# Kernel tuning notes

Measured on AMD Instinct MI355X. Metric: run time of the kernel, lower is better.

## Reference

```python
import math
import jax, jax.numpy as jnp
import numpy as np

S, B, H = 2048, 1, 4096
NH, HD = 32, 128          # heads, head dim
ROT = HD // 2             # rotary dim per 2D-RoPE half = 64


def rotate_half(x):
    x1, x2 = jnp.split(x, 2, axis=-1)
    return jnp.concatenate([-x2, x1], axis=-1)


def rope_tables(seq_len, dim, base=10000.0):
    inv_freq = 1.0 / (base ** (jnp.arange(0, dim, 2, dtype=jnp.float32) / dim))
    freqs = jnp.arange(seq_len, dtype=jnp.float32)[:, None] * inv_freq[None, :]
    emb = jnp.concatenate([freqs, freqs], axis=-1)  # [S, dim]
    return jnp.cos(emb), jnp.sin(emb)


def apply_rope(q, k, cos, sin, pos):
    # q,k: [S,B,NH,ROT]; pos: [S,B] -> gather cos/sin per token
    c = cos[pos][:, :, None, :]  # [S,B,1,ROT]
    s = sin[pos][:, :, None, :]
    return q * c + rotate_half(q) * s, k * c + rotate_half(k) * s


def setup_inputs() -> dict:
    key = jax.random.key(0)
    ks = jax.random.split(key, 5)
    hidden_states = jax.random.normal(ks[0], (S, B, H), dtype=jnp.float32)
    pos = jnp.arange(S, dtype=jnp.int64 if jax.config.jax_enable_x64 else jnp.int32)
    position_ids = jnp.stack([pos, pos])[None]  # [B=1, 2, S]
    attention_mask = jnp.triu(jnp.ones((S, S), dtype=bool), k=1)[None, None]  # True = masked
    scale = 0.02
    wqkv = jax.random.normal(ks[1], (3 * H, H), dtype=jnp.float32) * scale
    bqkv = jax.random.normal(ks[2], (3 * H,), dtype=jnp.float32) * scale
    wdense = jax.random.normal(ks[3], (H, H), dtype=jnp.float32) * scale
    bdense = jax.random.normal(ks[4], (H,), dtype=jnp.float32) * scale
    return {"hidden_states": hidden_states, "position_ids": position_ids,
            "attention_mask": attention_mask, "wqkv": wqkv, "bqkv": bqkv,
            "wdense": wdense, "bdense": bdense, "layer_id": 1}


def reference(hidden_states, position_ids, attention_mask, wqkv, bqkv, wdense, bdense, layer_id):
    s, b, h = hidden_states.shape
    # fused QKV projection: [S,B,NH,3*HD]
    mixed = (jnp.einsum('sbh,oh->sbo', hidden_states, wqkv) + bqkv).reshape(s, b, NH, 3 * HD)
    q, k, v = jnp.split(mixed, 3, axis=-1)  # each [S,B,NH,HD]

    # 2D RoPE: split head dim in half, rotate each half with its own position ids
    q1, q2 = jnp.split(q, 2, axis=-1)
    k1, k2 = jnp.split(k, 2, axis=-1)
    cos, sin = rope_tables(s, ROT)
    pos = position_ids[:, 0, :].T       # [S,B]
    block_pos = position_ids[:, 1, :].T  # [S,B]
    q1, k1 = apply_rope(q1, k1, cos, sin, pos)
    q2, k2 = apply_rope(q2, k2, cos, sin, block_pos)
    q = jnp.concatenate([q1, q2], axis=-1)
    k = jnp.concatenate([k1, k2], axis=-1)

    # layer-scaled attention (ChatGLM style)
    coeff = float(layer_id + 1)
    q = q / (math.sqrt(HD) * coeff)
    scores = jnp.einsum('sbhd,tbhd->bhst', q, k)  # [B,NH,S,S]
    scores = jnp.where(attention_mask, jnp.float32(-10000.0), scores)
    scores = scores.astype(jnp.float32) * coeff
    probs = jax.nn.softmax(scores, axis=-1).astype(q.dtype)
    context = jnp.einsum('bhst,tbhd->sbhd', probs, v).reshape(s, b, h)

    out = jnp.einsum('sbh,oh->sbo', context, wdense) + bdense
    return out
```

## Files before the change

### kernel.cpp

```cpp
#include <hip/hip_runtime.h>

typedef unsigned short u16;
typedef unsigned int u32;
typedef __attribute__((ext_vector_type(4))) float f32x4;
typedef __attribute__((ext_vector_type(16))) float f32x16;
typedef __attribute__((ext_vector_type(8))) short bf16x8;
typedef __attribute__((ext_vector_type(2))) unsigned int u32x2;

#define S_LEN 2048
#define NHEAD 32
#define HDD 128
#define HID 4096
#define N_QKV 12288
#define KDIM 4096
#define RS 12288

__device__ __forceinline__ u16 f2bf(float f) {
  u32 u = __builtin_bit_cast(u32, f);
  u = (u + 0x7FFFu + ((u >> 16) & 1u)) >> 16;
  return (u16)u;
}
__device__ __forceinline__ float bf2f(u16 h) {
  u32 u = ((u32)h) << 16;
  return __builtin_bit_cast(float, u);
}

__device__ __forceinline__ int gkey(int line) { return (line ^ (line >> 1)) & 7; }

__device__ __forceinline__ void gl2lds16(const void* g, void* l) {
  __builtin_amdgcn_global_load_lds(
      (const __attribute__((address_space(1))) u32*)g,
      (__attribute__((address_space(3))) u32*)l, 16, 0, 0);
}

#define FULL_BAR()                          \
  {                                         \
    asm volatile("" ::: "memory");          \
    __builtin_amdgcn_s_barrier();           \
    asm volatile("" ::: "memory");          \
  }

__global__ __launch_bounds__(256) void cvt3_kernel(const float* __restrict__ s0, u16* __restrict__ d0, int n0,
                                                   const float* __restrict__ s2, u16* __restrict__ d2, int n2,
                                                   float* __restrict__ cos_t, float* __restrict__ sin_t) {
  int i = blockIdx.x * blockDim.x + threadIdx.x;
  if (i < S_LEN * 32) {
    int s = i >> 5, ii = i & 31;
    float invf = expf(-0.28782313662425572f * (float)ii);
    float a = (float)s * invf;
    cos_t[i] = cosf(a);
    sin_t[i] = sinf(a);
  }
  int st = gridDim.x * blockDim.x;
  int ntot = n0 + n2;
  for (; i < ntot; i += st) {
    const float* s;
    u16* d;
    int j = i;
    if (j < n0) {
      s = s0; d = d0;
    } else {
      j -= n0; s = s2; d = d2;
    }
    float4 v = ((const float4*)s)[j];
    u32x2 o;
    o.x = (u32)f2bf(v.x) | ((u32)f2bf(v.y) << 16);
    o.y = (u32)f2bf(v.z) | ((u32)f2bf(v.w) << 16);
    ((u32x2*)d)[j] = o;
  }
}

__global__ __launch_bounds__(256) void ropek_kernel(u16* __restrict__ mixed,
                                                    const int* __restrict__ pid,
                                                    const float* __restrict__ cos_t,
                                                    const float* __restrict__ sin_t) {
  int idx = blockIdx.x * blockDim.x + threadIdx.x;
  const int total = NHEAD * S_LEN * 2 * 8;
  if (idx >= total) return;
  int j = idx & 7;
  int half = (idx >> 3) & 1;
  int s = (idx >> 4) & (S_LEN - 1);
  int h = idx >> 15;
  int i0 = j * 4;
  int p = pid[half * S_LEN + s];
  float4 c4 = *(const float4*)(cos_t + p * 32 + i0);
  float4 s4 = *(const float4*)(sin_t + p * 32 + i0);
  u16* base = mixed + (size_t)s * RS + h * 384 + 128 + half * 64 + i0;
  ushort4 x1v = *(const ushort4*)(base);
  ushort4 x2v = *(const ushort4*)(base + 32);
  ushort4 o1, o2;
  {
    float x1 = bf2f(x1v.x), x2 = bf2f(x2v.x);
    o1.x = f2bf(x1 * c4.x - x2 * s4.x);
    o2.x = f2bf(x2 * c4.x + x1 * s4.x);
  }
  {
    float x1 = bf2f(x1v.y), x2 = bf2f(x2v.y);
    o1.y = f2bf(x1 * c4.y - x2 * s4.y);
    o2.y = f2bf(x2 * c4.y + x1 * s4.y);
  }
  {
    float x1 = bf2f(x1v.z), x2 = bf2f(x2v.z);
    o1.z = f2bf(x1 * c4.z - x2 * s4.z);
    o2.z = f2bf(x2 * c4.z + x1 * s4.z);
  }
  {
    float x1 = bf2f(x1v.w), x2 = bf2f(x2v.w);
    o1.w = f2bf(x1 * c4.w - x2 * s4.w);
    o2.w = f2bf(x2 * c4.w + x1 * s4.w);
  }
  *(ushort4*)(base) = o1;
  *(ushort4*)(base + 32) = o2;
}

__global__ __launch_bounds__(512, 2) void gemmQ(const u16* __restrict__ A,
                                                const u16* __restrict__ B,
                                                const float* __restrict__ bias,
                                                u16* __restrict__ outb) {
  __shared__ __align__(16) char lds[3][40960];

  const int tid = threadIdx.x;
  const int lane = tid & 63, w = tid >> 6;
  const int l31 = lane & 31, hh = lane >> 5;
  const int wm = w >> 2, wn = w & 3;

  int x = blockIdx.x & 7, loc = blockIdx.x >> 3;
  int mb = loc & 7, nb = x * 4 + (loc >> 3);
  const int bm = mb * 256, bn = nb * 384;

  f32x16 acc[4][3];
#pragma unroll
  for (int mi = 0; mi < 4; ++mi)
#pragma unroll
    for (int ni = 0; ni < 3; ++ni)
#pragma unroll
      for (int r = 0; r < 16; ++r) acc[mi][ni][r] = 0.f;

  const size_t K2 = (size_t)KDIM * 2;

  const char* gA[2];
#pragma unroll
  for (int j = 0; j < 2; ++j) {
    int slot = j * 512 + tid;
    int line = slot >> 3;
    int sl = (slot & 7) ^ gkey(line);
    int row = 2 * line + (sl >> 2);
    int colb = (sl & 3) * 16;
    gA[j] = (const char*)A + (size_t)(bm + row) * K2 + colb;
  }
  const char* gB[3];
#pragma unroll
  for (int j = 0; j < 3; ++j) {
    int slot = j * 512 + tid;
    int line = slot >> 3;
    int sl = (slot & 7) ^ gkey(line);
    int row = 2 * line + (sl >> 2);
    int colb = (sl & 3) * 16;
    gB[j] = (const char*)B + (size_t)(bn + row) * K2 + colb;
  }
  const int ldst = w * 1024;

#define QIA(t, bi)                                                  \
  {                                                                 \
    char* Lb = lds[bi];                                             \
    gl2lds16(gA[0] + (size_t)(t) * 64, Lb + ldst);                  \
    gl2lds16(gA[1] + (size_t)(t) * 64, Lb + 8192 + ldst);           \
  }
#define QIB(t, bi)                                                  \
  {                                                                 \
    char* Lb = lds[bi] + 16384;                                     \
    _Pragma("unroll")                                               \
    for (int j = 0; j < 3; ++j)                                     \
      gl2lds16(gB[j] + (size_t)(t) * 64, Lb + j * 8192 + ldst);     \
  }

  int offA[4][2], offB[3][2];
#pragma unroll
  for (int mi = 0; mi < 4; ++mi) {
    int r = wm * 128 + mi * 32 + l31;
    int line = r >> 1;
#pragma unroll
    for (int kk = 0; kk < 2; ++kk) {
      int sl = (((r & 1) << 2) + kk * 2 + hh) ^ gkey(line);
      offA[mi][kk] = line * 128 + sl * 16;
    }
  }
#pragma unroll
  for (int ni = 0; ni < 3; ++ni) {
    int r = wn * 96 + ni * 32 + l31;
    int line = r >> 1;
#pragma unroll
    for (int kk = 0; kk < 2; ++kk) {
      int sl = (((r & 1) << 2) + kk * 2 + hh) ^ gkey(line);
      offB[ni][kk] = 16384 + line * 128 + sl * 16;
    }
  }

  QIA(0, 0); QIB(0, 0);
  QIA(1, 1); QIB(1, 1);
  asm volatile("s_waitcnt vmcnt(5)" ::: "memory");
  FULL_BAR();

  int cur = 0, nx2 = 2;
  for (int kt = 0; kt < 128; ++kt) {
    const char* buf = lds[cur];
    const bool pf = (kt + 2) < 128;
    bf16x8 a[4], b[3];
#pragma unroll
    for (int mi = 0; mi < 4; ++mi) a[mi] = *(const bf16x8*)(buf + offA[mi][0]);
#pragma unroll
    for (int ni = 0; ni < 3; ++ni) b[ni] = *(const bf16x8*)(buf + offB[ni][0]);
    if (pf) QIA(kt + 2, nx2);
    FULL_BAR();
    __builtin_amdgcn_s_setprio(1);
#pragma unroll
    for (int mi = 0; mi < 4; ++mi)
#pragma unroll
      for (int ni = 0; ni < 3; ++ni)
        acc[mi][ni] = __builtin_amdgcn_mfma_f32_32x32x16_bf16(a[mi], b[ni], acc[mi][ni], 0, 0, 0);
    __builtin_amdgcn_s_setprio(0);
#pragma unroll
    for (int mi = 0; mi < 4; ++mi) a[mi] = *(const bf16x8*)(buf + offA[mi][1]);
#pragma unroll
    for (int ni = 0; ni < 3; ++ni) b[ni] = *(const bf16x8*)(buf + offB[ni][1]);
    if (pf) {
      QIB(kt + 2, nx2);
      asm volatile("s_waitcnt vmcnt(5)" ::: "memory");
    } else if (kt == 126) {
      asm volatile("s_waitcnt vmcnt(0)" ::: "memory");
    }
    FULL_BAR();
    __builtin_amdgcn_s_setprio(1);
#pragma unroll
    for (int mi = 0; mi < 4; ++mi)
#pragma unroll
      for (int ni = 0; ni < 3; ++ni)
        acc[mi][ni] = __builtin_amdgcn_mfma_f32_32x32x16_bf16(a[mi], b[ni], acc[mi][ni], 0, 0, 0);
    __builtin_amdgcn_s_setprio(0);
    cur = (cur + 1 == 3) ? 0 : cur + 1;
    nx2 = (nx2 + 1 == 3) ? 0 : nx2 + 1;
  }
#undef QIA
#undef QIB

#pragma unroll
  for (int ni = 0; ni < 3; ++ni) {
    int n = bn + wn * 96 + ni * 32 + l31;
    float bv = bias[n];
#pragma unroll
    for (int mi = 0; mi < 4; ++mi) {
      int m0 = bm + wm * 128 + mi * 32 + 4 * hh;
#pragma unroll
      for (int reg = 0; reg < 16; ++reg) {
        int row = m0 + (reg & 3) + 8 * (reg >> 2);
        outb[(size_t)row * N_QKV + n] = f2bf(acc[mi][ni][reg] + bv);
      }
    }
  }
}

__global__ __launch_bounds__(512, 2) void gemmD(const u16* __restrict__ A,
                                                const float* __restrict__ Bf,
                                                const float* __restrict__ bias,
                                                float* __restrict__ outf) {
  __shared__ __align__(16) char lds[2][49152];

  const int tid = threadIdx.x;
  const int lane = tid & 63, w = tid >> 6;
  const int l31 = lane & 31, hh = lane >> 5;
  const int wm = w >> 1, wn = w & 1;

  int x = blockIdx.x & 7, loc = blockIdx.x >> 3;
  int mb = loc & 7, nb = x * 4 + (loc >> 3);
  const int bm = mb * 256, bn = nb * 128;

  f32x16 acc[2][2];
#pragma unroll
  for (int mi = 0; mi < 2; ++mi)
#pragma unroll
    for (int ni = 0; ni < 2; ++ni)
#pragma unroll
      for (int r = 0; r < 16; ++r) acc[mi][ni][r] = 0.f;

  const size_t K2 = (size_t)KDIM * 2;

  const char* gA[2];
#pragma unroll
  for (int j = 0; j < 2; ++j) {
    int slot = j * 512 + tid;
    int line = slot >> 3;
    int sl = (slot & 7) ^ gkey(line);
    int row = 2 * line + (sl >> 2);
    int colb = (sl & 3) * 16;
    gA[j] = (const char*)A + (size_t)(bm + row) * K2 + colb;
  }
  int bline = tid >> 3;
  int bsl = tid & 7;
  int brow = 2 * bline + (bsl >> 2);
  int bcole = (bsl & 3) * 8;
  const float* gBs = Bf + (size_t)(bn + brow) * KDIM + bcole;
  int bphys = bsl ^ gkey(bline);
  const int bwr = 32768 + bline * 128 + bphys * 16;
  const int ldst = w * 1024;

#define DIA(t, kk)                                                            \
  {                                                                           \
    char* Lb = lds[(t) & 1] + (kk) * 16384;                                   \
    gl2lds16(gA[0] + (size_t)(t) * 128 + (kk) * 64, Lb + ldst);               \
    gl2lds16(gA[1] + (size_t)(t) * 128 + (kk) * 64, Lb + 8192 + ldst);        \
  }
#define DGB(t)                                                                \
  {                                                                           \
    const float* p0 = gBs + (size_t)(t) * 64;                                 \
    b0a = *(const float4*)(p0);                                               \
    b0b = *(const float4*)(p0 + 4);                                           \
    b1a = *(const float4*)(p0 + 32);                                          \
    b1b = *(const float4*)(p0 + 36);                                          \
  }
#define DWB(t)                                                                \
  {                                                                           \
    bf16x8 o0, o1;                                                            \
    o0[0] = (short)f2bf(b0a.x); o0[1] = (short)f2bf(b0a.y);                   \
    o0[2] = (short)f2bf(b0a.z); o0[3] = (short)f2bf(b0a.w);                   \
    o0[4] = (short)f2bf(b0b.x); o0[5] = (short)f2bf(b0b.y);                   \
    o0[6] = (short)f2bf(b0b.z); o0[7] = (short)f2bf(b0b.w);                   \
    o1[0] = (short)f2bf(b1a.x); o1[1] = (short)f2bf(b1a.y);                   \
    o1[2] = (short)f2bf(b1a.z); o1[3] = (short)f2bf(b1a.w);                   \
    o1[4] = (short)f2bf(b1b.x); o1[5] = (short)f2bf(b1b.y);                   \
    o1[6] = (short)f2bf(b1b.z); o1[7] = (short)f2bf(b1b.w);                   \
    char* Lb = lds[(t) & 1];                                                  \
    *(bf16x8*)(Lb + bwr) = o0;                                                \
    *(bf16x8*)(Lb + 8192 + bwr) = o1;                                         \
  }

  int offA[2][2][2], offB[2][2][2];
#pragma unroll
  for (int mi = 0; mi < 2; ++mi) {
    int r = wm * 64 + mi * 32 + l31;
    int line = r >> 1;
#pragma unroll
    for (int kku = 0; kku < 2; ++kku)
#pragma unroll
      for (int st = 0; st < 2; ++st) {
        int sl = (((r & 1) << 2) + st * 2 + hh) ^ gkey(line);
        offA[mi][kku][st] = kku * 16384 + line * 128 + sl * 16;
      }
  }
#pragma unroll
  for (int ni = 0; ni < 2; ++ni) {
    int r = wn * 64 + ni * 32 + l31;
    int line = r >> 1;
#pragma unroll
    for (int kku = 0; kku < 2; ++kku)
#pragma unroll
      for (int st = 0; st < 2; ++st) {
        int sl = (((r & 1) << 2) + st * 2 + hh) ^ gkey(line);
        offB[ni][kku][st] = 32768 + kku * 8192 + line * 128 + sl * 16;
      }
  }

  float4 b0a, b0b, b1a, b1b;
  DGB(0);
  DIA(0, 0);
  DIA(0, 1);
  asm volatile("s_waitcnt vmcnt(4)" ::: "memory");
  DWB(0);
  asm volatile("s_waitcnt vmcnt(0) lgkmcnt(0)" ::: "memory");
  FULL_BAR();

  for (int kt = 0; kt < 64; ++kt) {
    const char* buf = lds[kt & 1];
    const bool pf = (kt + 1) < 64;
    bf16x8 a[2][2], b[2][2];
#pragma unroll
    for (int mi = 0; mi < 2; ++mi)
#pragma unroll
      for (int st = 0; st < 2; ++st) a[mi][st] = *(const bf16x8*)(buf + offA[mi][0][st]);
#pragma unroll
    for (int ni = 0; ni < 2; ++ni)
#pragma unroll
      for (int st = 0; st < 2; ++st) b[ni][st] = *(const bf16x8*)(buf + offB[ni][0][st]);
    if (pf) {
      DIA(kt + 1, 0);
      DGB(kt + 1);
      asm volatile("s_waitcnt vmcnt(6)" ::: "memory");
    } else {
      asm volatile("s_waitcnt vmcnt(0)" ::: "memory");
    }
    FULL_BAR();
    __builtin_amdgcn_s_setprio(1);
#pragma unroll
    for (int st = 0; st < 2; ++st)
#pragma unroll
      for (int mi = 0; mi < 2; ++mi)
#pragma unroll
        for (int ni = 0; ni < 2; ++ni)
          acc[mi][ni] = __builtin_amdgcn_mfma_f32_32x32x16_bf16(a[mi][st], b[ni][st], acc[mi][ni], 0, 0, 0);
    __builtin_amdgcn_s_setprio(0);
#pragma unroll
    for (int mi = 0; mi < 2; ++mi)
#pragma unroll
      for (int st = 0; st < 2; ++st) a[mi][st] = *(const bf16x8*)(buf + offA[mi][1][st]);
#pragma unroll
    for (int ni = 0; ni < 2; ++ni)
#pragma unroll
      for (int st = 0; st < 2; ++st) b[ni][st] = *(const bf16x8*)(buf + offB[ni][1][st]);
    if (pf) {
      DIA(kt + 1, 1);
      asm volatile("s_waitcnt vmcnt(2)" ::: "memory");
      DWB(kt + 1);
      asm volatile("s_waitcnt lgkmcnt(0)" ::: "memory");
    }
    FULL_BAR();
    __builtin_amdgcn_s_setprio(1);
#pragma unroll
    for (int st = 0; st < 2; ++st)
#pragma unroll
      for (int mi = 0; mi < 2; ++mi)
#pragma unroll
        for (int ni = 0; ni < 2; ++ni)
          acc[mi][ni] = __builtin_amdgcn_mfma_f32_32x32x16_bf16(a[mi][st], b[ni][st], acc[mi][ni], 0, 0, 0);
    __builtin_amdgcn_s_setprio(0);
  }
#undef DIA
#undef DGB
#undef DWB

#pragma unroll
  for (int ni = 0; ni < 2; ++ni) {
    int n = bn + wn * 64 + ni * 32 + l31;
    float bv = bias[n];
#pragma unroll
    for (int mi = 0; mi < 2; ++mi) {
      int m0 = bm + wm * 64 + mi * 32 + 4 * hh;
#pragma unroll
      for (int reg = 0; reg < 16; ++reg) {
        int row = m0 + (reg & 3) + 8 * (reg >> 2);
        outf[(size_t)row * HID + n] = acc[mi][ni][reg] + bv;
      }
    }
  }
}

__global__ __launch_bounds__(256) void attn_kernel(const u16* __restrict__ mixed,
                                                   const int* __restrict__ pid,
                                                   const float* __restrict__ cos_t,
                                                   const float* __restrict__ sin_t,
                                                   u16* __restrict__ ctx) {
  __shared__ __align__(16) u16 Ksh[64 * 136];
  __shared__ __align__(16) u16 Vsh[128 * 64];
  __shared__ __align__(16) u16 Pt[4][16 * 72];

  int tid = threadIdx.x;
  int lane = tid & 63, w = tid >> 6;
  int lane15 = lane & 15, g = lane >> 4;

  int bpair = blockIdx.x & 15;
  int h = blockIdx.x >> 4;

  const u16* qp = mixed + (size_t)h * 384;
  const u16* kp = mixed + (size_t)h * 384 + 128;
  const u16* vp = mixed + (size_t)h * 384 + 256;

  int krow = tid >> 2, kc = (tid & 3) * 32;
  int vk0 = 2 * (tid & 31), vd0 = (tid >> 5) * 16;
  f32x4 z4 = {0.f, 0.f, 0.f, 0.f};
  const float QSC = 0.08838834764831845f;
  const float L2E = 1.4426950408889634f;

  for (int pass = 0; pass < 2; ++pass) {
    int qi = pass ? (31 - bpair) : bpair;
    int qbase = qi * 64;
    int qrow = qbase + w * 16 + lane15;
    int ntiles = qi + 1;

    bf16x8 qf[4];
    const u16* qptr = qp + (size_t)qrow * RS + g * 8;
#pragma unroll
    for (int d0 = 0; d0 < 4; ++d0) qf[d0] = *(const bf16x8*)(qptr + d0 * 32);
    {
      int p1 = pid[qrow], p2 = pid[S_LEN + qrow];
      float cc[8], ss[8], dd[8], tt[8];
#pragma unroll
      for (int j = 0; j < 8; ++j) {
        cc[j] = cos_t[p1 * 32 + g * 8 + j];
        ss[j] = sin_t[p1 * 32 + g * 8 + j];
        dd[j] = cos_t[p2 * 32 + g * 8 + j];
        tt[j] = sin_t[p2 * 32 + g * 8 + j];
      }
#pragma unroll
      for (int j = 0; j < 8; ++j) {
        float x1 = bf2f((u16)qf[0][j]), x2 = bf2f((u16)qf[1][j]);
        qf[0][j] = (short)f2bf((x1 * cc[j] - x2 * ss[j]) * QSC);
        qf[1][j] = (short)f2bf((x2 * cc[j] + x1 * ss[j]) * QSC);
        float y1 = bf2f((u16)qf[2][j]), y2 = bf2f((u16)qf[3][j]);
        qf[2][j] = (short)f2bf((y1 * dd[j] - y2 * tt[j]) * QSC);
        qf[3][j] = (short)f2bf((y2 * dd[j] + y1 * tt[j]) * QSC);
      }
    }

    f32x4 pv[8];
#pragma unroll
    for (int db = 0; db < 8; ++db) pv[db] = z4;
    float m_run = -1e30f, l_run = 0.0f;

    for (int t = 0; t < ntiles; ++t) {
      int kb0 = t * 64;
      __syncthreads();
      {
        const bf16x8* src = (const bf16x8*)(kp + (size_t)(kb0 + krow) * RS + kc);
#pragma unroll
        for (int c = 0; c < 4; ++c)
          *(bf16x8*)(Ksh + krow * 136 + kc + c * 8) = src[c];
        const bf16x8* r0p = (const bf16x8*)(vp + (size_t)(kb0 + vk0) * RS + vd0);
        const bf16x8* r1p = (const bf16x8*)(vp + (size_t)(kb0 + vk0 + 1) * RS + vd0);
        bf16x8 r00 = r0p[0], r01 = r0p[1];
        bf16x8 r10 = r1p[0], r11 = r1p[1];
#pragma unroll
        for (int jj = 0; jj < 8; ++jj) {
          int d = vd0 + jj;
          u32 v0 = (u32)(u16)r00[jj] | ((u32)(u16)r10[jj] << 16);
          *(u32*)((char*)Vsh + d * 128 + (((vk0 >> 3) ^ (d & 7)) << 4) + (vk0 & 7) * 2) = v0;
          int d2 = vd0 + 8 + jj;
          u32 v1 = (u32)(u16)r01[jj] | ((u32)(u16)r11[jj] << 16);
          *(u32*)((char*)Vsh + d2 * 128 + (((vk0 >> 3) ^ (d2 & 7)) << 4) + (vk0 & 7) * 2) = v1;
        }
      }
      __syncthreads();

      f32x4 sa[4];
#pragma unroll
      for (int kt16 = 0; kt16 < 4; ++kt16) sa[kt16] = z4;
#pragma unroll
      for (int kt16 = 0; kt16 < 4; ++kt16)
#pragma unroll
        for (int d0 = 0; d0 < 4; ++d0) {
          bf16x8 kf = *(const bf16x8*)(Ksh + (kt16 * 16 + lane15) * 136 + d0 * 32 + g * 8);
          sa[kt16] = __builtin_amdgcn_mfma_f32_16x16x32_bf16(kf, qf[d0], sa[kt16], 0, 0, 0);
        }
      float s[16];
#pragma unroll
      for (int kt16 = 0; kt16 < 4; ++kt16)
#pragma unroll
        for (int rr = 0; rr < 4; ++rr) {
          int kg = kb0 + kt16 * 16 + 4 * g + rr;
          s[kt16 * 4 + rr] = (kg > qrow) ? -1e30f : sa[kt16][rr];
        }
      float mx = s[0];
#pragma unroll
      for (int i2 = 1; i2 < 16; ++i2) mx = fmaxf(mx, s[i2]);
      mx = fmaxf(mx, __shfl_xor(mx, 16));
      mx = fmaxf(mx, __shfl_xor(mx, 32));
      float mnew = fmaxf(m_run, mx);
      float fac = exp2f((m_run - mnew) * L2E);
      float p[16], psum = 0.f;
#pragma unroll
      for (int i2 = 0; i2 < 16; ++i2) {
        p[i2] = exp2f((s[i2] - mnew) * L2E);
        psum += p[i2];
      }
      psum += __shfl_xor(psum, 16);
      psum += __shfl_xor(psum, 32);
      l_run = l_run * fac + psum;
      m_run = mnew;
#pragma unroll
      for (int db = 0; db < 8; ++db) pv[db] *= fac;

#pragma unroll
      for (int kt16 = 0; kt16 < 4; ++kt16) {
        u32x2 pw;
        pw.x = (u32)f2bf(p[kt16 * 4 + 0]) | ((u32)f2bf(p[kt16 * 4 + 1]) << 16);
        pw.y = (u32)f2bf(p[kt16 * 4 + 2]) | ((u32)f2bf(p[kt16 * 4 + 3]) << 16);
        *(u32x2*)(&Pt[w][lane15 * 72 + kt16 * 16 + 4 * g]) = pw;
      }
      asm volatile("s_waitcnt lgkmcnt(0)" ::: "memory");
      bf16x8 pf0 = *(const bf16x8*)(&Pt[w][lane15 * 72 + 8 * g]);
      bf16x8 pf1 = *(const bf16x8*)(&Pt[w][lane15 * 72 + 32 + 8 * g]);

#pragma unroll
      for (int db = 0; db < 8; ++db) {
        int d = db * 16 + lane15;
        bf16x8 vf0 = *(const bf16x8*)((const char*)Vsh + d * 128 + ((g ^ (d & 7)) << 4));
        bf16x8 vf1 = *(const bf16x8*)((const char*)Vsh + d * 128 + (((4 + g) ^ (d & 7)) << 4));
        pv[db] = __builtin_amdgcn_mfma_f32_16x16x32_bf16(vf0, pf0, pv[db], 0, 0, 0);
        pv[db] = __builtin_amdgcn_mfma_f32_16x16x32_bf16(vf1, pf1, pv[db], 0, 0, 0);
      }
    }

    float inv = 1.0f / l_run;
#pragma unroll
    for (int db = 0; db < 8; ++db) {
      ushort4 o;
      o.x = f2bf(pv[db][0] * inv);
      o.y = f2bf(pv[db][1] * inv);
      o.z = f2bf(pv[db][2] * inv);
      o.w = f2bf(pv[db][3] * inv);
      *(ushort4*)(ctx + (size_t)qrow * HID + h * HDD + db * 16 + 4 * g) = o;
    }
    __syncthreads();
  }
}

extern "C" void kernel_launch(void* const* d_in, const int* in_sizes, int n_in,
                              void* d_out, int out_size, void* d_ws, size_t ws_size,
                              hipStream_t stream) {
  const float* hidden = (const float*)d_in[0];
  const int* pid = (const int*)d_in[1];
  const float* wqkv = (const float*)d_in[3];
  const float* bqkv = (const float*)d_in[4];
  const float* wdense = (const float*)d_in[5];
  const float* bdense = (const float*)d_in[6];
  float* out = (float*)d_out;

  char* ws = (char*)d_ws;
  u16* W1 = (u16*)ws;
  u16* X = (u16*)(ws + 134217728);
  u16* mixed = (u16*)(ws + 150994944);
  u16* ctx = (u16*)(ws + 201326592);
  float* cos_t = (float*)(ws + 218103808);
  float* sin_t = (float*)(ws + 218365952);

  cvt3_kernel<<<dim3(2048), dim3(256), 0, stream>>>(
      wqkv, W1, N_QKV * KDIM / 4, hidden, X, S_LEN * HID / 4, cos_t, sin_t);

  gemmQ<<<dim3(256), dim3(512), 0, stream>>>(X, W1, bqkv, mixed);

  ropek_kernel<<<dim3(4096), dim3(256), 0, stream>>>(mixed, pid, cos_t, sin_t);

  attn_kernel<<<dim3(512), dim3(256), 0, stream>>>(mixed, pid, cos_t, sin_t, ctx);

  gemmD<<<dim3(256), dim3(512), 0, stream>>>(ctx, wdense, bdense, out);
}
```

Baseline: 483.1 us.

## Double-buffer K/V tiles, widen attention blocks to 8 waves, lazy softmax rescale

The attention kernel now runs 512-thread blocks that each handle two adjacent 64-row query tiles. K/V tiles are shared across both tiles and double-buffered in LDS, with the next tile's global loads issued before the current tile's compute, so each iteration needs one barrier instead of two. The online softmax also skips rescaling the running max and accumulators unless some lane's max grows by more than a threshold. The lower query tile in each pair does redundant masked work on the final K tile. Grid halves to 256 blocks and LDS usage roughly doubles.

After: 453.9 us. -6.1%, faster.

```diff
diff --git a/kernel.cpp b/kernel.cpp
--- a/kernel.cpp
+++ b/kernel.cpp
@@ -442,37 +442,59 @@
   }
 }
 
-__global__ __launch_bounds__(256) void attn_kernel(const u16* __restrict__ mixed,
+__global__ __launch_bounds__(512) void attn_kernel(const u16* __restrict__ mixed,
                                                    const int* __restrict__ pid,
                                                    const float* __restrict__ cos_t,
                                                    const float* __restrict__ sin_t,
                                                    u16* __restrict__ ctx) {
-  __shared__ __align__(16) u16 Ksh[64 * 136];
-  __shared__ __align__(16) u16 Vsh[128 * 64];
-  __shared__ __align__(16) u16 Pt[4][16 * 72];
+  __shared__ __align__(16) u16 Ksh[2][64 * 136];
+  __shared__ __align__(16) u16 Vsh[2][128 * 64];
+  __shared__ __align__(16) u16 Pt[8][16 * 72];
 
   int tid = threadIdx.x;
   int lane = tid & 63, w = tid >> 6;
   int lane15 = lane & 15, g = lane >> 4;
 
-  int bpair = blockIdx.x & 15;
-  int h = blockIdx.x >> 4;
+  int bpg = blockIdx.x & 7;
+  int h = blockIdx.x >> 3;
 
   const u16* qp = mixed + (size_t)h * 384;
   const u16* kp = mixed + (size_t)h * 384 + 128;
   const u16* vp = mixed + (size_t)h * 384 + 256;
 
-  int krow = tid >> 2, kc = (tid & 3) * 32;
-  int vk0 = 2 * (tid & 31), vd0 = (tid >> 5) * 16;
+  int krow = tid >> 3, kc = (tid & 7) * 16;
+  int vk0 = 2 * (tid & 31), vd0 = (tid >> 5) * 8;
   f32x4 z4 = {0.f, 0.f, 0.f, 0.f};
   const float QSC = 0.08838834764831845f;
   const float L2E = 1.4426950408889634f;
 
+  bf16x8 kx0, kx1, vr0, vr1;
+#define ALOAD(t)                                                              \
+  {                                                                           \
+    const u16* kr = kp + (size_t)((t)*64 + krow) * RS + kc;                   \
+    kx0 = *(const bf16x8*)kr;                                                 \
+    kx1 = *(const bf16x8*)(kr + 8);                                           \
+    const u16* vr = vp + (size_t)((t)*64 + vk0) * RS + vd0;                   \
+    vr0 = *(const bf16x8*)vr;                                                 \
+    vr1 = *(const bf16x8*)(vr + RS);                                          \
+  }
+#define AWRITE(bb)                                                            \
+  {                                                                           \
+    *(bf16x8*)(&Ksh[bb][krow * 136 + kc]) = kx0;                              \
+    *(bf16x8*)(&Ksh[bb][krow * 136 + kc + 8]) = kx1;                          \
+    _Pragma("unroll") for (int jj = 0; jj < 8; ++jj) {                        \
+      int d = vd0 + jj;                                                       \
+      u32 val = (u32)(u16)vr0[jj] | ((u32)(u16)vr1[jj] << 16);                \
+      *(u32*)((char*)Vsh[bb] + d * 128 + (((vk0 >> 3) ^ (d & 7)) << 4) +      \
+              (vk0 & 7) * 2) = val;                                           \
+    }                                                                         \
+  }
+
   for (int pass = 0; pass < 2; ++pass) {
-    int qi = pass ? (31 - bpair) : bpair;
-    int qbase = qi * 64;
-    int qrow = qbase + w * 16 + lane15;
-    int ntiles = qi + 1;
+    int pg = pass ? (15 - bpg) : bpg;
+    int qi = 2 * pg + (w >> 2);
+    int qrow = qi * 64 + (w & 3) * 16 + lane15;
+    int ntiles = 2 * pg + 2;
 
     bf16x8 qf[4];
     const u16* qptr = qp + (size_t)qrow * RS + g * 8;
@@ -504,30 +526,16 @@
     for (int db = 0; db < 8; ++db) pv[db] = z4;
     float m_run = -1e30f, l_run = 0.0f;
 
+    ALOAD(0);
+    AWRITE(0);
+    __syncthreads();
+
     for (int t = 0; t < ntiles; ++t) {
+      const u16* Kc = Ksh[t & 1];
+      const char* Vc = (const char*)Vsh[t & 1];
+      if (t + 1 < ntiles) ALOAD(t + 1);
+
       int kb0 = t * 64;
-      __syncthreads();
-      {
-        const bf16x8* src = (const bf16x8*)(kp + (size_t)(kb0 + krow) * RS + kc);
-#pragma unroll
-        for (int c = 0; c < 4; ++c)
-          *(bf16x8*)(Ksh + krow * 136 + kc + c * 8) = src[c];
-        const bf16x8* r0p = (const bf16x8*)(vp + (size_t)(kb0 + vk0) * RS + vd0);
-        const bf16x8* r1p = (const bf16x8*)(vp + (size_t)(kb0 + vk0 + 1) * RS + vd0);
-        bf16x8 r00 = r0p[0], r01 = r0p[1];
-        bf16x8 r10 = r1p[0], r11 = r1p[1];
-#pragma unroll
-        for (int jj = 0; jj < 8; ++jj) {
-          int d = vd0 + jj;
-          u32 v0 = (u32)(u16)r00[jj] | ((u32)(u16)r10[jj] << 16);
-          *(u32*)((char*)Vsh + d * 128 + (((vk0 >> 3) ^ (d & 7)) << 4) + (vk0 & 7) * 2) = v0;
-          int d2 = vd0 + 8 + jj;
-          u32 v1 = (u32)(u16)r01[jj] | ((u32)(u16)r11[jj] << 16);
-          *(u32*)((char*)Vsh + d2 * 128 + (((vk0 >> 3) ^ (d2 & 7)) << 4) + (vk0 & 7) * 2) = v1;
-        }
-      }
-      __syncthreads();
-
       f32x4 sa[4];
 #pragma unroll
       for (int kt16 = 0; kt16 < 4; ++kt16) sa[kt16] = z4;
@@ -535,7 +543,7 @@
       for (int kt16 = 0; kt16 < 4; ++kt16)
 #pragma unroll
         for (int d0 = 0; d0 < 4; ++d0) {
-          bf16x8 kf = *(const bf16x8*)(Ksh + (kt16 * 16 + lane15) * 136 + d0 * 32 + g * 8);
+          bf16x8 kf = *(const bf16x8*)(Kc + (kt16 * 16 + lane15) * 136 + d0 * 32 + g * 8);
           sa[kt16] = __builtin_amdgcn_mfma_f32_16x16x32_bf16(kf, qf[d0], sa[kt16], 0, 0, 0);
         }
       float s[16];
@@ -551,20 +559,23 @@
       for (int i2 = 1; i2 < 16; ++i2) mx = fmaxf(mx, s[i2]);
       mx = fmaxf(mx, __shfl_xor(mx, 16));
       mx = fmaxf(mx, __shfl_xor(mx, 32));
-      float mnew = fmaxf(m_run, mx);
-      float fac = exp2f((m_run - mnew) * L2E);
+      if (!__all(mx - m_run <= 8.0f)) {
+        float mnew = fmaxf(m_run, mx);
+        float fac = exp2f((m_run - mnew) * L2E);
+        l_run *= fac;
+#pragma unroll
+        for (int db = 0; db < 8; ++db) pv[db] *= fac;
+        m_run = mnew;
+      }
       float p[16], psum = 0.f;
 #pragma unroll
       for (int i2 = 0; i2 < 16; ++i2) {
-        p[i2] = exp2f((s[i2] - mnew) * L2E);
+        p[i2] = exp2f((s[i2] - m_run) * L2E);
         psum += p[i2];
       }
       psum += __shfl_xor(psum, 16);
       psum += __shfl_xor(psum, 32);
-      l_run = l_run * fac + psum;
-      m_run = mnew;
-#pragma unroll
-      for (int db = 0; db < 8; ++db) pv[db] *= fac;
+      l_run += psum;
 
 #pragma unroll
       for (int kt16 = 0; kt16 < 4; ++kt16) {
@@ -580,11 +591,14 @@
 #pragma unroll
       for (int db = 0; db < 8; ++db) {
         int d = db * 16 + lane15;
-        bf16x8 vf0 = *(const bf16x8*)((const char*)Vsh + d * 128 + ((g ^ (d & 7)) << 4));
-        bf16x8 vf1 = *(const bf16x8*)((const char*)Vsh + d * 128 + (((4 + g) ^ (d & 7)) << 4));
+        bf16x8 vf0 = *(const bf16x8*)(Vc + d * 128 + ((g ^ (d & 7)) << 4));
+        bf16x8 vf1 = *(const bf16x8*)(Vc + d * 128 + (((4 + g) ^ (d & 7)) << 4));
         pv[db] = __builtin_amdgcn_mfma_f32_16x16x32_bf16(vf0, pf0, pv[db], 0, 0, 0);
         pv[db] = __builtin_amdgcn_mfma_f32_16x16x32_bf16(vf1, pf1, pv[db], 0, 0, 0);
       }
+
+      if (t + 1 < ntiles) AWRITE((t + 1) & 1);
+      __syncthreads();
     }
 
     float inv = 1.0f / l_run;
@@ -599,6 +613,8 @@
     }
     __syncthreads();
   }
+#undef ALOAD
+#undef AWRITE
 }
 
 extern "C" void kernel_launch(void* const* d_in, const int* in_sizes, int n_in,
@@ -627,7 +643,7 @@
 
   ropek_kernel<<<dim3(4096), dim3(256), 0, stream>>>(mixed, pid, cos_t, sin_t);
 
-  attn_kernel<<<dim3(512), dim3(256), 0, stream>>>(mixed, pid, cos_t, sin_t, ctx);
+  attn_kernel<<<dim3(256), dim3(512), 0, stream>>>(mixed, pid, cos_t, sin_t, ctx);
 
   gemmD<<<dim3(256), dim3(512), 0, stream>>>(ctx, wdense, bdense, out);
 }
```
